# Kernel optimization log

Hardware: AMD Instinct MI355X
Metric: run time of the kernel (lower is better)

Reference implementation:

```python
import jax, jax.numpy as jnp
import numpy as np

N, E, F_IN, D, K, OUT = 50000, 800000, 16, 64, 3, 3


def _safe_dinv(deg):
    safe = jnp.where(deg > 0, deg, 1.0)
    return jnp.where(deg > 0, jax.lax.rsqrt(safe), 0.0)


def _gcn(x, src, dst, W, b, n):
    # GCNConv(improved=True): A_hat = A + 2I, sym normalization
    xw = x @ W
    ones = jnp.ones(src.shape[0], x.dtype)
    deg = jax.ops.segment_sum(ones, dst, num_segments=n) + 2.0  # self-loop weight 2
    dinv = jax.lax.rsqrt(deg)  # deg >= 2, always finite
    agg = jax.ops.segment_sum((dinv[src] * dinv[dst])[:, None] * xw[src], dst, num_segments=n)
    agg = agg + (2.0 * dinv * dinv)[:, None] * xw  # self-loop contribution
    return agg + b


def _cheb(x, src, dst, dinv, W, b, n):
    # ChebConv, normalization='sym', lambda_max=2.0  =>  L_hat = -D^{-1/2} A D^{-1/2}
    coef = (dinv[src] * dinv[dst])[:, None]

    def lhat(z):
        return -jax.ops.segment_sum(coef * z[src], dst, num_segments=n)

    z_prev = x
    out = x @ W[0]
    z_cur = lhat(x)
    out = out + z_cur @ W[1]
    for k in range(2, W.shape[0]):
        z_next = 2.0 * lhat(z_cur) - z_prev
        out = out + z_next @ W[k]
        z_prev, z_cur = z_cur, z_next
    return out + b


def _gclstm(x, H, C, src, dst, dinv, wx, bx, wh, bh, wc, bg, n):
    # gate order in stacks: [i, f, c, o]; peephole wc: [i, f, o]
    gx = lambda g: _cheb(x, src, dst, dinv, wx[g], bx[g], n)
    gh = lambda g: _cheb(H, src, dst, dinv, wh[g], bh[g], n)
    i = jax.nn.sigmoid(gx(0) + gh(0) + wc[0] * C + bg[0])
    f = jax.nn.sigmoid(gx(1) + gh(1) + wc[1] * C + bg[1])
    t = jnp.tanh(gx(2) + gh(2) + bg[2])
    Cn = f * C + i * t
    o = jax.nn.sigmoid(gx(3) + gh(3) + wc[2] * Cn + bg[3])
    return o * jnp.tanh(Cn), Cn


def _forward(x, edge_index, p):
    (w_gcn1, b_gcn1, w_gcn2, b_gcn2,
     wx1, bx1, wh1, bh1, wc1, bg1,
     wx2, bx2, wh2, bh2, wc2, bg2,
     wx3, bx3, wh3, bh3, wc3, bg3,
     lin_w, lin_b) = p
    src, dst = edge_index[0], edge_index[1]
    n = x.shape[0]
    ones = jnp.ones(src.shape[0], x.dtype)
    deg_c = jax.ops.segment_sum(ones, dst, num_segments=n)  # Cheb: no self loops
    dinv_c = _safe_dinv(deg_c)

    h = jax.nn.relu(_gcn(x, src, dst, w_gcn1, b_gcn1, n))
    h = jax.nn.relu(_gcn(h, src, dst, w_gcn2, b_gcn2, n))

    z = jnp.zeros((n, wh1.shape[-1]), h.dtype)  # H=C=None -> zeros per cell
    H1, _ = _gclstm(h, z, z, src, dst, dinv_c, wx1, bx1, wh1, bh1, wc1, bg1, n)
    H2, _ = _gclstm(H1, z, z, src, dst, dinv_c, wx2, bx2, wh2, bh2, wc2, bg2, n)
    H3, _ = _gclstm(H2, z, z, src, dst, dinv_c, wx3, bx3, wh3, bh3, wc3, bg3, n)
    return jax.nn.relu(H3) @ lin_w + lin_b


def setup_inputs() -> dict:
    key = jax.random.key(0)

    def nrm(i, shape):
        return 0.1 * jax.random.normal(jax.random.fold_in(key, i), shape, jnp.float32)

    inp = {}
    inp["x"] = jax.random.normal(jax.random.fold_in(key, 0), (N, F_IN), jnp.float32)
    inp["edge_index"] = jax.random.randint(jax.random.fold_in(key, 1), (2, E), 0, N)
    inp["w_gcn1"] = nrm(2, (F_IN, D))
    inp["b_gcn1"] = nrm(3, (D,))
    inp["w_gcn2"] = nrm(4, (D, D))
    inp["b_gcn2"] = nrm(5, (D,))
    i = 6
    for l in (1, 2, 3):
        inp[f"wx{l}"] = nrm(i, (4, K, D, D)); i += 1
        inp[f"bx{l}"] = nrm(i, (4, D)); i += 1
        inp[f"wh{l}"] = nrm(i, (4, K, D, D)); i += 1
        inp[f"bh{l}"] = nrm(i, (4, D)); i += 1
        inp[f"wc{l}"] = nrm(i, (3, D)); i += 1
        inp[f"bg{l}"] = nrm(i, (4, D)); i += 1
    inp["lin_w"] = nrm(i, (D, OUT))
    inp["lin_b"] = nrm(i + 1, (OUT,))
    return inp


def reference(x, edge_index, w_gcn1, b_gcn1, w_gcn2, b_gcn2,
              wx1, bx1, wh1, bh1, wc1, bg1,
              wx2, bx2, wh2, bh2, wc2, bg2,
              wx3, bx3, wh3, bh3, wc3, bg3,
              lin_w, lin_b):
    p = (w_gcn1, b_gcn1, w_gcn2, b_gcn2,
         wx1, bx1, wh1, bh1, wc1, bg1,
         wx2, bx2, wh2, bh2, wc2, bg2,
         wx3, bx3, wh3, bh3, wc3, bg3,
         lin_w, lin_b)
    return _forward(x, edge_index, p)
```

## Files before the change

kernel.cpp:

```cpp
#include <hip/hip_runtime.h>


typedef _Float16 half8 __attribute__((ext_vector_type(8)));
typedef float f32x4 __attribute__((ext_vector_type(4)));

__global__ void prep_kernel(const float* __restrict__ wx0, const float* __restrict__ wx1,
                            const float* __restrict__ wx2, const float* __restrict__ Wg2,
                            _Float16* __restrict__ Wpk, _Float16* __restrict__ Wpk2,
                            int* __restrict__ cursor, int n) {
  int idx = blockIdx.x * 256 + threadIdx.x;
  if (idx < 110592) {
    int l = idx / 36864;
    int r = idx % 36864;
    int g = r / 12288;
    int r2 = r % 12288;
    int k = r2 / 64;
    int nn = r2 % 64;
    const float* wx = (l == 0) ? wx0 : (l == 1 ? wx1 : wx2);
    int gs = (g == 0) ? 0 : (g == 1 ? 2 : 3);
    int tau = k >> 6, kd = k & 63;
    size_t base = ((size_t)gs * 3) * 4096 + (size_t)kd * 64 + nn;
    float v;
    if (tau == 0)      v = wx[base] - wx[base + 2 * 4096];
    else if (tau == 1) v = wx[base + 1 * 4096];
    else               v = 2.f * wx[base + 2 * 4096];
    int kc = k >> 5, klo = k & 31;
    int lane = ((klo >> 3) << 4) | (nn & 15);
    int j = klo & 7;
    int nt = nn >> 4;
    Wpk[((((size_t)l * 3 + g) * 6 + kc) * 4 + nt) * 512 + (size_t)lane * 8 + j] = (_Float16)v;
  } else if (idx < 114688) {
    int i2 = idx - 110592;
    int k = i2 >> 6, nn = i2 & 63;
    float v = Wg2[k * 64 + nn];
    int kc = k >> 5, klo = k & 31;
    int lane = ((klo >> 3) << 4) | (nn & 15);
    int j = klo & 7;
    int nt = nn >> 4;
    Wpk2[(((size_t)kc * 4 + nt) * 64 + lane) * 8 + j] = (_Float16)v;
  } else if (idx < 114688 + n) {
    int i = idx - 114688;
    cursor[i] = i << 6;
  }
}

__global__ void fill_x_kernel(const int* __restrict__ ei, int* __restrict__ cursor,
                              unsigned short* __restrict__ csr, int E, int chunk) {
  int range = blockIdx.x & 7;
  int lo = range * chunk, hi = lo + chunk;
  int stride = (gridDim.x >> 3) * blockDim.x;
  for (int e = (blockIdx.x >> 3) * blockDim.x + threadIdx.x; e < E; e += stride) {
    int d = ei[E + e];
    if (d >= lo && d < hi) {
      int pos = atomicAdd(&cursor[d], 1);
      if (pos < ((d + 1) << 6)) csr[pos] = (unsigned short)ei[e];
    }
  }
}

__global__ void post_kernel(const int* __restrict__ cursor, int* __restrict__ deg,
                            float* __restrict__ dg, float* __restrict__ dc,
                            float* __restrict__ rc,
                            const float* __restrict__ x, _Float16* __restrict__ x16s,
                            int n, int nsbN) {
  int tid = threadIdx.x;
  if ((int)blockIdx.x < nsbN) {
    int i = blockIdx.x * 256 + tid;
    if (i < n) {
      int v = cursor[i] - (i << 6);
      deg[i] = (v > 64) ? 64 : v;
      dg[i] = rsqrtf((float)v + 2.f);
      dc[i] = (v > 0) ? rsqrtf((float)v) : 0.f;
      rc[i] = (v > 0) ? sqrtf((float)v) : 0.f;
    }
  } else {
    int i = (blockIdx.x - nsbN) * 256 + tid;
    if (i < n * 16) {
      int node = i >> 4;
      int v = cursor[node] - (node << 6);
      x16s[i] = (_Float16)(rsqrtf((float)v + 2.f) * x[i]);
    }
  }
}

__global__ __launch_bounds__(256) void gcn1_fused_kernel(
    const _Float16* __restrict__ X16s, const float* __restrict__ W1,
    const float* __restrict__ b1, const float* __restrict__ dg,
    _Float16* __restrict__ OUTs,
    const int* __restrict__ deg, const unsigned short* __restrict__ csr, int n) {
  __shared__ float w1s[16 * 64];
  int tid = threadIdx.x;
  for (int i = tid; i < 1024; i += 256) w1s[i] = W1[i];
  __syncthreads();
  int node = blockIdx.x * 8 + (tid >> 5);
  if (node >= n) return;
  int lane = tid & 63;
  int l32 = tid & 31;
  int eg = l32 >> 1, c8 = l32 & 1;
  int beg = node << 6, dgg = deg[node];
  const half8* IN8 = (const half8*)X16s;
  int idx = 0;
  if (l32 < dgg) idx = csr[beg + l32];
  float acc[8];
#pragma unroll
  for (int j = 0; j < 8; ++j) acc[j] = 0.f;
  int kmaxU = (dgg + 15) >> 4; if (kmaxU > 2) kmaxU = 2;
  for (int k = 0; k < kmaxU; ++k) {
    int s = __shfl(idx, eg + 16 * k, 32);
    half8 v = IN8[(size_t)s * 2 + c8];
    if (eg + 16 * k < dgg) {
#pragma unroll
      for (int j = 0; j < 8; ++j) acc[j] += (float)v[j];
    }
  }
  for (int p = beg + eg + 32; p < beg + dgg; p += 16) {
    int s = csr[p];
    half8 v = IN8[(size_t)s * 2 + c8];
#pragma unroll
    for (int j = 0; j < 8; ++j) acc[j] += (float)v[j];
  }
#pragma unroll
  for (int j = 0; j < 8; ++j) {
    acc[j] += __shfl_xor(acc[j], 2);
    acc[j] += __shfl_xor(acc[j], 4);
    acc[j] += __shfl_xor(acc[j], 8);
    acc[j] += __shfl_xor(acc[j], 16);
  }
  float dt = dg[node];
  half8 self = IN8[(size_t)node * 2 + c8];
  float v8[8];
#pragma unroll
  for (int j = 0; j < 8; ++j) v8[j] = dt * acc[j] + 2.f * dt * (float)self[j];
  float agg[16];
  int base = lane & 32;
#pragma unroll
  for (int k = 0; k < 16; ++k) agg[k] = __shfl(v8[k & 7], base + (k >> 3));
  float h0 = b1[l32], h1 = b1[l32 + 32];
#pragma unroll
  for (int k = 0; k < 16; ++k) {
    h0 += agg[k] * w1s[k * 64 + l32];
    h1 += agg[k] * w1s[k * 64 + l32 + 32];
  }
  OUTs[(size_t)node * 64 + l32]      = (_Float16)(dt * fmaxf(h0, 0.f));
  OUTs[(size_t)node * 64 + l32 + 32] = (_Float16)(dt * fmaxf(h1, 0.f));
}

template <int MODE>
__global__ void gather_kernel(const int* __restrict__ deg,
                              const unsigned short* __restrict__ csr,
                              const float* __restrict__ dinv,
                              const _Float16* __restrict__ INs,
                              _Float16* __restrict__ OUT, int n) {
  int node = blockIdx.x * (blockDim.x >> 6) + (threadIdx.x >> 6);
  if (node >= n) return;
  int lane = threadIdx.x & 63;
  int eg = lane >> 3, c8 = lane & 7;
  int beg = node << 6, dgg = deg[node];
  const half8* IN8 = (const half8*)INs;
  int idx = 0;
  if (lane < dgg) idx = csr[beg + lane];
  float acc[8], acc2[8];
#pragma unroll
  for (int j = 0; j < 8; ++j) { acc[j] = 0.f; acc2[j] = 0.f; }
  int kmaxU = (dgg + 7) >> 3;
  int k = 0;
  for (; k + 2 <= kmaxU; k += 2) {
    int s0 = __shfl(idx, eg + 8 * k);
    int s1 = __shfl(idx, eg + 8 * k + 8);
    half8 v0 = IN8[(size_t)s0 * 8 + c8];
    half8 v1 = IN8[(size_t)s1 * 8 + c8];
    if (eg + 8 * k < dgg) {
#pragma unroll
      for (int j = 0; j < 8; ++j) acc[j] += (float)v0[j];
    }
    if (eg + 8 * k + 8 < dgg) {
#pragma unroll
      for (int j = 0; j < 8; ++j) acc2[j] += (float)v1[j];
    }
  }
  if (k < kmaxU) {
    int s = __shfl(idx, eg + 8 * k);
    half8 v = IN8[(size_t)s * 8 + c8];
    if (eg + 8 * k < dgg) {
#pragma unroll
      for (int j = 0; j < 8; ++j) acc[j] += (float)v[j];
    }
  }
#pragma unroll
  for (int j = 0; j < 8; ++j) {
    acc[j] += acc2[j];
    acc[j] += __shfl_xor(acc[j], 8);
    acc[j] += __shfl_xor(acc[j], 16);
    acc[j] += __shfl_xor(acc[j], 32);
  }
  if (eg == 0) {
    float dt = dinv[node];
    size_t o8 = (size_t)node * 8 + c8;
    half8 r;
    if (MODE == 0) {
      half8 self = IN8[o8];
#pragma unroll
      for (int j = 0; j < 8; ++j) r[j] = (_Float16)(dt * acc[j] + 2.f * dt * (float)self[j]);
    } else if (MODE == 1) {
      float s = -dt * dt;
#pragma unroll
      for (int j = 0; j < 8; ++j) r[j] = (_Float16)(s * acc[j]);
    } else {
#pragma unroll
      for (int j = 0; j < 8; ++j) r[j] = (_Float16)(-dt * acc[j]);
    }
    ((half8*)OUT)[o8] = r;
  }
}

__global__ __launch_bounds__(256) void gcn2_mfma_kernel(
    const _Float16* __restrict__ A, const _Float16* __restrict__ W2,
    const float* __restrict__ bias, const float* __restrict__ dc,
    _Float16* __restrict__ OUT, _Float16* __restrict__ OUTs, int n) {
  int tid = threadIdx.x;
  int wid = tid >> 6, lane = tid & 63;
  int n0 = blockIdx.x * 64;
  int row = n0 + wid * 16 + (lane & 15);
  int rowc = min(row, n - 1);
  int ksub = (lane >> 4) << 3;
  int dbase = lane & 15;
  const _Float16* Wlane = W2 + (size_t)lane * 8;
  f32x4 acc[4];
#pragma unroll
  for (int nt = 0; nt < 4; ++nt) {
    float b = bias[nt * 16 + dbase];
    acc[nt] = (f32x4){b, b, b, b};
  }
#pragma unroll
  for (int kc = 0; kc < 2; ++kc) {
    half8 a = *(const half8*)&A[(size_t)rowc * 64 + (kc << 5) + ksub];
#pragma unroll
    for (int nt = 0; nt < 4; ++nt) {
      half8 b = *(const half8*)(Wlane + (size_t)(kc * 4 + nt) * 512);
      acc[nt] = __builtin_amdgcn_mfma_f32_16x16x32_f16(a, b, acc[nt], 0, 0, 0);
    }
  }
  int mrow = n0 + wid * 16 + ((lane >> 4) << 2);
#pragma unroll
  for (int nt = 0; nt < 4; ++nt) {
    int d = nt * 16 + dbase;
#pragma unroll
    for (int r = 0; r < 4; ++r) {
      int node = mrow + r;
      if (node < n) {
        float h = fmaxf(acc[nt][r], 0.f);
        OUT[(size_t)node * 64 + d] = (_Float16)h;
        OUTs[(size_t)node * 64 + d] = (_Float16)(dc[node] * h);
      }
    }
  }
}

template <int FINAL>
__global__ __launch_bounds__(256) void gate_mfma_kernel(
    const _Float16* __restrict__ X, const _Float16* __restrict__ Z1s,
    const _Float16* __restrict__ Y,
    const _Float16* __restrict__ Wl,
    const float* __restrict__ bx, const float* __restrict__ bh, const float* __restrict__ bg,
    const float* __restrict__ wc, const float* __restrict__ dc,
    const float* __restrict__ rinv,
    _Float16* __restrict__ H, _Float16* __restrict__ Hs,
    const float* __restrict__ lw, const float* __restrict__ lb,
    float* __restrict__ out, int n) {
  int tid = threadIdx.x;
  int wid = tid >> 6, lane = tid & 63;
  int n0 = blockIdx.x * 64;
  int row = n0 + wid * 16 + (lane & 15);
  int rowc = min(row, n - 1);
  int ksub = (lane >> 4) << 3;
  const _Float16* Wlane = Wl + (size_t)lane * 8;
  int dbase = lane & 15;
  float rv = rinv[rowc];

  f32x4 acc[3][4];
#pragma unroll
  for (int g = 0; g < 3; ++g) {
    int gs = (g == 0) ? 0 : (g == 1 ? 2 : 3);
#pragma unroll
    for (int nt = 0; nt < 4; ++nt) {
      int d = nt * 16 + dbase;
      float b = bx[gs * 64 + d] + bh[gs * 64 + d] + bg[gs * 64 + d];
      acc[g][nt] = (f32x4){b, b, b, b};
    }
  }
  const _Float16* T[3] = {X, Z1s, Y};
#pragma unroll
  for (int kc = 0; kc < 6; ++kc) {
    const _Float16* t = T[kc >> 1];
    half8 a = *(const half8*)&t[(size_t)rowc * 64 + ((kc & 1) << 5) + ksub];
    if (kc >= 2 && kc < 4) {
#pragma unroll
      for (int j = 0; j < 8; ++j) a[j] = (_Float16)((float)a[j] * rv);
    }
#pragma unroll
    for (int g = 0; g < 3; ++g) {
#pragma unroll
      for (int nt = 0; nt < 4; ++nt) {
        half8 b = *(const half8*)(Wlane + (size_t)((g * 6 + kc) * 4 + nt) * 512);
        acc[g][nt] = __builtin_amdgcn_mfma_f32_16x16x32_f16(a, b, acc[g][nt], 0, 0, 0);
      }
    }
  }
  int mrow = n0 + wid * 16 + ((lane >> 4) << 2);
  float po[4][3];
  if (FINAL) {
#pragma unroll
    for (int r = 0; r < 4; ++r) { po[r][0] = 0.f; po[r][1] = 0.f; po[r][2] = 0.f; }
  }
#pragma unroll
  for (int nt = 0; nt < 4; ++nt) {
    int d = nt * 16 + dbase;
    float wcd = wc[128 + d];
#pragma unroll
    for (int r = 0; r < 4; ++r) {
      float ig = 1.f / (1.f + expf(-acc[0][nt][r]));
      float tt = tanhf(acc[1][nt][r]);
      float Cn = ig * tt;
      float og = 1.f / (1.f + expf(-(acc[2][nt][r] + wcd * Cn)));
      float h = og * tanhf(Cn);
      if (FINAL) {
        float rl = fmaxf(h, 0.f);
        po[r][0] += rl * lw[d * 3 + 0];
        po[r][1] += rl * lw[d * 3 + 1];
        po[r][2] += rl * lw[d * 3 + 2];
      } else {
        int node = mrow + r;
        if (node < n) {
          H[(size_t)node * 64 + d] = (_Float16)h;
          Hs[(size_t)node * 64 + d] = (_Float16)(dc[node] * h);
        }
      }
    }
  }
  if (FINAL) {
#pragma unroll
    for (int m = 1; m < 16; m <<= 1) {
#pragma unroll
      for (int r = 0; r < 4; ++r) {
        po[r][0] += __shfl_xor(po[r][0], m);
        po[r][1] += __shfl_xor(po[r][1], m);
        po[r][2] += __shfl_xor(po[r][2], m);
      }
    }
    if (dbase == 0) {
#pragma unroll
      for (int r = 0; r < 4; ++r) {
        int node = mrow + r;
        if (node < n) {
          out[(size_t)node * 3 + 0] = po[r][0] + lb[0];
          out[(size_t)node * 3 + 1] = po[r][1] + lb[1];
          out[(size_t)node * 3 + 2] = po[r][2] + lb[2];
        }
      }
    }
  }
}

extern "C" void kernel_launch(void* const* d_in, const int* in_sizes, int n_in,
                              void* d_out, int out_size, void* d_ws, size_t ws_size,
                              hipStream_t stream) {
  const float* x      = (const float*)d_in[0];
  const int*   ei     = (const int*)d_in[1];
  const float* w_gcn1 = (const float*)d_in[2];
  const float* b_gcn1 = (const float*)d_in[3];
  const float* w_gcn2 = (const float*)d_in[4];
  const float* b_gcn2 = (const float*)d_in[5];
  const float* wx[3]  = {(const float*)d_in[6],  (const float*)d_in[12], (const float*)d_in[18]};
  const float* bx[3]  = {(const float*)d_in[7],  (const float*)d_in[13], (const float*)d_in[19]};
  const float* bh[3]  = {(const float*)d_in[9],  (const float*)d_in[15], (const float*)d_in[21]};
  const float* wc[3]  = {(const float*)d_in[10], (const float*)d_in[16], (const float*)d_in[22]};
  const float* bg[3]  = {(const float*)d_in[11], (const float*)d_in[17], (const float*)d_in[23]};
  const float* lin_w  = (const float*)d_in[24];
  const float* lin_b  = (const float*)d_in[25];
  float* out = (float*)d_out;

  int N = in_sizes[0] / 16;
  int E = in_sizes[1] / 2;
  int chunk = (N + 7) / 8;
  int nsbN = (N + 255) / 256;
  int nsbX = (N * 16 + 255) / 256;

  char* ws = (char*)d_ws;
  size_t off = 0;
  auto alloc = [&](size_t bytes) {
    void* p = ws + off;
    off = (off + bytes + 255) & ~(size_t)255;
    return p;
  };
  int* deg        = (int*)alloc((size_t)N * 4);
  int* cursor     = (int*)alloc((size_t)N * 4);
  unsigned short* csr = (unsigned short*)alloc((size_t)N * 64 * 2);
  float* dinv_g   = (float*)alloc((size_t)N * 4);
  float* dinv_c   = (float*)alloc((size_t)N * 4);
  float* rinv_c   = (float*)alloc((size_t)N * 4);
  _Float16* Wpk   = (_Float16*)alloc((size_t)3 * 36864 * 2);
  _Float16* Wpk2  = (_Float16*)alloc((size_t)4096 * 2);
  _Float16* x16s  = (_Float16*)alloc((size_t)N * 16 * 2);
  _Float16* bufA  = (_Float16*)alloc((size_t)N * 64 * 2);
  _Float16* bufAs = (_Float16*)alloc((size_t)N * 64 * 2);
  _Float16* bufB  = (_Float16*)alloc((size_t)N * 64 * 2);
  _Float16* bufC  = (_Float16*)alloc((size_t)N * 64 * 2);
  (void)ws_size; (void)n_in; (void)out_size;

  int nbw  = (N + 3) / 4;
  int nb64 = (N + 63) / 64;
  int nb8  = (N + 7) / 8;

  prep_kernel<<<(114688 + N + 255) / 256, 256, 0, stream>>>(wx[0], wx[1], wx[2], w_gcn2,
                                                            Wpk, Wpk2, cursor, N);
  fill_x_kernel<<<4096, 256, 0, stream>>>(ei, cursor, csr, E, chunk);
  post_kernel<<<nsbN + nsbX, 256, 0, stream>>>(cursor, deg, dinv_g, dinv_c, rinv_c,
                                               x, x16s, N, nsbN);

  gcn1_fused_kernel<<<nb8, 256, 0, stream>>>(x16s, w_gcn1, b_gcn1, dinv_g, bufB,
                                             deg, csr, N);
  gather_kernel<0><<<nbw, 256, 0, stream>>>(deg, csr, dinv_g, bufB, bufC, N);
  gcn2_mfma_kernel<<<nb64, 256, 0, stream>>>(bufC, Wpk2, b_gcn2, dinv_c, bufA, bufAs, N);

  for (int l = 0; l < 3; ++l) {
    gather_kernel<1><<<nbw, 256, 0, stream>>>(deg, csr, dinv_c, bufAs, bufB, N);
    gather_kernel<3><<<nbw, 256, 0, stream>>>(deg, csr, dinv_c, bufB, bufC, N);
    if (l < 2) {
      gate_mfma_kernel<0><<<nb64, 256, 0, stream>>>(bufA, bufB, bufC, Wpk + (size_t)l * 36864,
                                                    bx[l], bh[l], bg[l], wc[l], dinv_c, rinv_c,
                                                    bufA, bufAs, nullptr, nullptr, nullptr, N);
    } else {
      gate_mfma_kernel<1><<<nb64, 256, 0, stream>>>(bufA, bufB, bufC, Wpk + (size_t)l * 36864,
                                                    bx[l], bh[l], bg[l], wc[l], dinv_c, rinv_c,
                                                    nullptr, nullptr, lin_w, lin_b, out, N);
    }
  }
}
```

Measured before the change: 305.5 us.

## Split node feature buffers into lo/hi column halves for gather locality

Stores the 64-channel fp16 node features as two separate 32-channel arrays and has each gather launch handle one half per block set. Each random-access gather pass then touches a smaller contiguous array, which is meant to improve cache hit rates for neighbour reads. The cost is duplicated CSR/degree reads, one extra shuffle-reduce stage, and split stores and loads in the GCN and gate kernels.

Measured after the change: 420.3 us. +37.6%, slower.

```diff
diff --git a/kernel.cpp b/kernel.cpp
--- a/kernel.cpp
+++ b/kernel.cpp
@@ -86,7 +86,7 @@
 __global__ __launch_bounds__(256) void gcn1_fused_kernel(
     const _Float16* __restrict__ X16s, const float* __restrict__ W1,
     const float* __restrict__ b1, const float* __restrict__ dg,
-    _Float16* __restrict__ OUTs,
+    _Float16* __restrict__ OUTlo, _Float16* __restrict__ OUThi,
     const int* __restrict__ deg, const unsigned short* __restrict__ csr, int n) {
   __shared__ float w1s[16 * 64];
   int tid = threadIdx.x;
@@ -141,47 +141,54 @@
     h0 += agg[k] * w1s[k * 64 + l32];
     h1 += agg[k] * w1s[k * 64 + l32 + 32];
   }
-  OUTs[(size_t)node * 64 + l32]      = (_Float16)(dt * fmaxf(h0, 0.f));
-  OUTs[(size_t)node * 64 + l32 + 32] = (_Float16)(dt * fmaxf(h1, 0.f));
+  OUTlo[(size_t)node * 32 + l32] = (_Float16)(dt * fmaxf(h0, 0.f));
+  OUThi[(size_t)node * 32 + l32] = (_Float16)(dt * fmaxf(h1, 0.f));
 }
 
 template <int MODE>
 __global__ void gather_kernel(const int* __restrict__ deg,
                               const unsigned short* __restrict__ csr,
                               const float* __restrict__ dinv,
-                              const _Float16* __restrict__ INs,
-                              _Float16* __restrict__ OUT, int n) {
-  int node = blockIdx.x * (blockDim.x >> 6) + (threadIdx.x >> 6);
+                              const _Float16* __restrict__ IN_lo,
+                              const _Float16* __restrict__ IN_hi,
+                              _Float16* __restrict__ OUT_lo,
+                              _Float16* __restrict__ OUT_hi, int n, int nbh) {
+  int bid = blockIdx.x;
+  int half = (bid >= nbh) ? 1 : 0;
+  if (half) bid -= nbh;
+  const _Float16* INs = half ? IN_hi : IN_lo;
+  _Float16* OUT = half ? OUT_hi : OUT_lo;
+  int node = bid * (blockDim.x >> 6) + (threadIdx.x >> 6);
   if (node >= n) return;
   int lane = threadIdx.x & 63;
-  int eg = lane >> 3, c8 = lane & 7;
-  int beg = node << 6, dgg = deg[node];
+  int eg = lane >> 2, c8 = lane & 3;
+  int dgg = deg[node];
   const half8* IN8 = (const half8*)INs;
   int idx = 0;
-  if (lane < dgg) idx = csr[beg + lane];
+  if (lane < dgg) idx = csr[(node << 6) + lane];
   float acc[8], acc2[8];
 #pragma unroll
   for (int j = 0; j < 8; ++j) { acc[j] = 0.f; acc2[j] = 0.f; }
-  int kmaxU = (dgg + 7) >> 3;
+  int kmaxU = (dgg + 15) >> 4;
   int k = 0;
   for (; k + 2 <= kmaxU; k += 2) {
-    int s0 = __shfl(idx, eg + 8 * k);
-    int s1 = __shfl(idx, eg + 8 * k + 8);
-    half8 v0 = IN8[(size_t)s0 * 8 + c8];
-    half8 v1 = IN8[(size_t)s1 * 8 + c8];
-    if (eg + 8 * k < dgg) {
+    int s0 = __shfl(idx, eg + 16 * k);
+    int s1 = __shfl(idx, eg + 16 * k + 16);
+    half8 v0 = IN8[(size_t)s0 * 4 + c8];
+    half8 v1 = IN8[(size_t)s1 * 4 + c8];
+    if (eg + 16 * k < dgg) {
 #pragma unroll
       for (int j = 0; j < 8; ++j) acc[j] += (float)v0[j];
     }
-    if (eg + 8 * k + 8 < dgg) {
+    if (eg + 16 * k + 16 < dgg) {
 #pragma unroll
       for (int j = 0; j < 8; ++j) acc2[j] += (float)v1[j];
     }
   }
   if (k < kmaxU) {
-    int s = __shfl(idx, eg + 8 * k);
-    half8 v = IN8[(size_t)s * 8 + c8];
-    if (eg + 8 * k < dgg) {
+    int s = __shfl(idx, eg + 16 * k);
+    half8 v = IN8[(size_t)s * 4 + c8];
+    if (eg + 16 * k < dgg) {
 #pragma unroll
       for (int j = 0; j < 8; ++j) acc[j] += (float)v[j];
     }
@@ -189,16 +196,17 @@
 #pragma unroll
   for (int j = 0; j < 8; ++j) {
     acc[j] += acc2[j];
+    acc[j] += __shfl_xor(acc[j], 4);
     acc[j] += __shfl_xor(acc[j], 8);
     acc[j] += __shfl_xor(acc[j], 16);
     acc[j] += __shfl_xor(acc[j], 32);
   }
   if (eg == 0) {
     float dt = dinv[node];
-    size_t o8 = (size_t)node * 8 + c8;
+    size_t o = (size_t)node * 4 + c8;
     half8 r;
     if (MODE == 0) {
-      half8 self = IN8[o8];
+      half8 self = IN8[o];
 #pragma unroll
       for (int j = 0; j < 8; ++j) r[j] = (_Float16)(dt * acc[j] + 2.f * dt * (float)self[j]);
     } else if (MODE == 1) {
@@ -209,14 +217,16 @@
 #pragma unroll
       for (int j = 0; j < 8; ++j) r[j] = (_Float16)(-dt * acc[j]);
     }
-    ((half8*)OUT)[o8] = r;
+    ((half8*)OUT)[o] = r;
   }
 }
 
 __global__ __launch_bounds__(256) void gcn2_mfma_kernel(
-    const _Float16* __restrict__ A, const _Float16* __restrict__ W2,
+    const _Float16* __restrict__ Alo, const _Float16* __restrict__ Ahi,
+    const _Float16* __restrict__ W2,
     const float* __restrict__ bias, const float* __restrict__ dc,
-    _Float16* __restrict__ OUT, _Float16* __restrict__ OUTs, int n) {
+    _Float16* __restrict__ OUT, _Float16* __restrict__ OUTs_lo,
+    _Float16* __restrict__ OUTs_hi, int n) {
   int tid = threadIdx.x;
   int wid = tid >> 6, lane = tid & 63;
   int n0 = blockIdx.x * 64;
@@ -233,7 +243,8 @@
   }
 #pragma unroll
   for (int kc = 0; kc < 2; ++kc) {
-    half8 a = *(const half8*)&A[(size_t)rowc * 64 + (kc << 5) + ksub];
+    const _Float16* t = kc ? Ahi : Alo;
+    half8 a = *(const half8*)&t[(size_t)rowc * 32 + ksub];
 #pragma unroll
     for (int nt = 0; nt < 4; ++nt) {
       half8 b = *(const half8*)(Wlane + (size_t)(kc * 4 + nt) * 512);
@@ -250,7 +261,9 @@
       if (node < n) {
         float h = fmaxf(acc[nt][r], 0.f);
         OUT[(size_t)node * 64 + d] = (_Float16)h;
-        OUTs[(size_t)node * 64 + d] = (_Float16)(dc[node] * h);
+        float hs = dc[node] * h;
+        if (d < 32) OUTs_lo[(size_t)node * 32 + d] = (_Float16)hs;
+        else        OUTs_hi[(size_t)node * 32 + d - 32] = (_Float16)hs;
       }
     }
   }
@@ -258,13 +271,14 @@
 
 template <int FINAL>
 __global__ __launch_bounds__(256) void gate_mfma_kernel(
-    const _Float16* __restrict__ X, const _Float16* __restrict__ Z1s,
-    const _Float16* __restrict__ Y,
+    const _Float16* __restrict__ X,
+    const _Float16* __restrict__ Z1lo, const _Float16* __restrict__ Z1hi,
+    const _Float16* __restrict__ Ylo, const _Float16* __restrict__ Yhi,
     const _Float16* __restrict__ Wl,
     const float* __restrict__ bx, const float* __restrict__ bh, const float* __restrict__ bg,
     const float* __restrict__ wc, const float* __restrict__ dc,
     const float* __restrict__ rinv,
-    _Float16* __restrict__ H, _Float16* __restrict__ Hs,
+    _Float16* __restrict__ H, _Float16* __restrict__ Hs_lo, _Float16* __restrict__ Hs_hi,
     const float* __restrict__ lw, const float* __restrict__ lb,
     float* __restrict__ out, int n) {
   int tid = threadIdx.x;
@@ -288,11 +302,14 @@
       acc[g][nt] = (f32x4){b, b, b, b};
     }
   }
-  const _Float16* T[3] = {X, Z1s, Y};
 #pragma unroll
   for (int kc = 0; kc < 6; ++kc) {
-    const _Float16* t = T[kc >> 1];
-    half8 a = *(const half8*)&t[(size_t)rowc * 64 + ((kc & 1) << 5) + ksub];
+    half8 a;
+    if (kc < 2)      a = *(const half8*)&X[(size_t)rowc * 64 + ((kc & 1) << 5) + ksub];
+    else if (kc == 2) a = *(const half8*)&Z1lo[(size_t)rowc * 32 + ksub];
+    else if (kc == 3) a = *(const half8*)&Z1hi[(size_t)rowc * 32 + ksub];
+    else if (kc == 4) a = *(const half8*)&Ylo[(size_t)rowc * 32 + ksub];
+    else              a = *(const half8*)&Yhi[(size_t)rowc * 32 + ksub];
     if (kc >= 2 && kc < 4) {
 #pragma unroll
       for (int j = 0; j < 8; ++j) a[j] = (_Float16)((float)a[j] * rv);
@@ -332,7 +349,9 @@
         int node = mrow + r;
         if (node < n) {
           H[(size_t)node * 64 + d] = (_Float16)h;
-          Hs[(size_t)node * 64 + d] = (_Float16)(dc[node] * h);
+          float hs = dc[node] * h;
+          if (d < 32) Hs_lo[(size_t)node * 32 + d] = (_Float16)hs;
+          else        Hs_hi[(size_t)node * 32 + d - 32] = (_Float16)hs;
         }
       }
     }
@@ -401,13 +420,16 @@
   _Float16* Wpk   = (_Float16*)alloc((size_t)3 * 36864 * 2);
   _Float16* Wpk2  = (_Float16*)alloc((size_t)4096 * 2);
   _Float16* x16s  = (_Float16*)alloc((size_t)N * 16 * 2);
-  _Float16* bufA  = (_Float16*)alloc((size_t)N * 64 * 2);
-  _Float16* bufAs = (_Float16*)alloc((size_t)N * 64 * 2);
-  _Float16* bufB  = (_Float16*)alloc((size_t)N * 64 * 2);
-  _Float16* bufC  = (_Float16*)alloc((size_t)N * 64 * 2);
+  _Float16* bufA    = (_Float16*)alloc((size_t)N * 64 * 2);
+  _Float16* bufAsLo = (_Float16*)alloc((size_t)N * 32 * 2);
+  _Float16* bufAsHi = (_Float16*)alloc((size_t)N * 32 * 2);
+  _Float16* bufBLo  = (_Float16*)alloc((size_t)N * 32 * 2);
+  _Float16* bufBHi  = (_Float16*)alloc((size_t)N * 32 * 2);
+  _Float16* bufCLo  = (_Float16*)alloc((size_t)N * 32 * 2);
+  _Float16* bufCHi  = (_Float16*)alloc((size_t)N * 32 * 2);
   (void)ws_size; (void)n_in; (void)out_size;
 
-  int nbw  = (N + 3) / 4;
+  int nbh  = (N + 3) / 4;
   int nb64 = (N + 63) / 64;
   int nb8  = (N + 7) / 8;
 
@@ -417,22 +439,30 @@
   post_kernel<<<nsbN + nsbX, 256, 0, stream>>>(cursor, deg, dinv_g, dinv_c, rinv_c,
                                                x, x16s, N, nsbN);
 
-  gcn1_fused_kernel<<<nb8, 256, 0, stream>>>(x16s, w_gcn1, b_gcn1, dinv_g, bufB,
-                                             deg, csr, N);
-  gather_kernel<0><<<nbw, 256, 0, stream>>>(deg, csr, dinv_g, bufB, bufC, N);
-  gcn2_mfma_kernel<<<nb64, 256, 0, stream>>>(bufC, Wpk2, b_gcn2, dinv_c, bufA, bufAs, N);
+  gcn1_fused_kernel<<<nb8, 256, 0, stream>>>(x16s, w_gcn1, b_gcn1, dinv_g,
+                                             bufBLo, bufBHi, deg, csr, N);
+  gather_kernel<0><<<2 * nbh, 256, 0, stream>>>(deg, csr, dinv_g, bufBLo, bufBHi,
+                                                bufCLo, bufCHi, N, nbh);
+  gcn2_mfma_kernel<<<nb64, 256, 0, stream>>>(bufCLo, bufCHi, Wpk2, b_gcn2, dinv_c,
+                                             bufA, bufAsLo, bufAsHi, N);
 
   for (int l = 0; l < 3; ++l) {
-    gather_kernel<1><<<nbw, 256, 0, stream>>>(deg, csr, dinv_c, bufAs, bufB, N);
-    gather_kernel<3><<<nbw, 256, 0, stream>>>(deg, csr, dinv_c, bufB, bufC, N);
+    gather_kernel<1><<<2 * nbh, 256, 0, stream>>>(deg, csr, dinv_c, bufAsLo, bufAsHi,
+                                                  bufBLo, bufBHi, N, nbh);
+    gather_kernel<3><<<2 * nbh, 256, 0, stream>>>(deg, csr, dinv_c, bufBLo, bufBHi,
+                                                  bufCLo, bufCHi, N, nbh);
     if (l < 2) {
-      gate_mfma_kernel<0><<<nb64, 256, 0, stream>>>(bufA, bufB, bufC, Wpk + (size_t)l * 36864,
+      gate_mfma_kernel<0><<<nb64, 256, 0, stream>>>(bufA, bufBLo, bufBHi, bufCLo, bufCHi,
+                                                    Wpk + (size_t)l * 36864,
                                                     bx[l], bh[l], bg[l], wc[l], dinv_c, rinv_c,
-                                                    bufA, bufAs, nullptr, nullptr, nullptr, N);
+                                                    bufA, bufAsLo, bufAsHi,
+                                                    nullptr, nullptr, nullptr, N);
     } else {
-      gate_mfma_kernel<1><<<nb64, 256, 0, stream>>>(bufA, bufB, bufC, Wpk + (size_t)l * 36864,
+      gate_mfma_kernel<1><<<nb64, 256, 0, stream>>>(bufA, bufBLo, bufBHi, bufCLo, bufCHi,
+                                                    Wpk + (size_t)l * 36864,
                                                     bx[l], bh[l], bg[l], wc[l], dinv_c, rinv_c,
-                                                    nullptr, nullptr, lin_w, lin_b, out, N);
-    }
-  }
-}
+                                                    nullptr, nullptr, nullptr,
+                                                    lin_w, lin_b, out, N);
+    }
+  }
+}
```
